# Kernel optimization log

Hardware: AMD Instinct MI355X
Metric: run time of the kernel (lower is better)

Reference implementation:

```python
import jax, jax.numpy as jnp
import numpy as np
from jax import lax

N_QUBITS = 4


def _apply_ry(state, wire, theta):
    """Apply RY(theta) on `wire`. state: [N,2,2,2,2] real. theta: scalar or [N]."""
    theta = jnp.asarray(theta)
    if theta.ndim == 1:
        theta = theta.reshape(-1, 1, 1, 1)  # broadcast over remaining qubit axes
    s = jnp.moveaxis(state, 1 + wire, -1)
    c, sn = jnp.cos(theta / 2), jnp.sin(theta / 2)
    s0, s1 = s[..., 0], s[..., 1]
    s = jnp.stack([c * s0 - sn * s1, sn * s0 + c * s1], axis=-1)
    return jnp.moveaxis(s, -1, 1 + wire)


def _apply_cnot(state, ctrl, tgt):
    s = jnp.moveaxis(state, (1 + ctrl, 1 + tgt), (-2, -1))
    s = s.at[..., 1, :].set(s[..., 1, ::-1])
    return jnp.moveaxis(s, (-2, -1), (1 + ctrl, 1 + tgt))


def _quantum_filter(patches, angles):
    """patches: [N,4] rotation angles per qubit; returns PauliZ expectations [N,4]."""
    n = patches.shape[0]
    state = jnp.zeros((n, 2, 2, 2, 2), dtype=patches.dtype)
    state = state.at[:, 0, 0, 0, 0].set(1.0)  # |0000>
    # GeneralEncoder: RY(x_i) on wire i
    for w in range(N_QUBITS):
        state = _apply_ry(state, w, patches[:, w])
    # fixed 8-op random layer: 5 RY (learned angles) + 3 CNOTs
    state = _apply_ry(state, 0, angles[0])
    state = _apply_ry(state, 1, angles[1])
    state = _apply_cnot(state, 0, 1)
    state = _apply_ry(state, 2, angles[2])
    state = _apply_cnot(state, 1, 2)
    state = _apply_ry(state, 3, angles[3])
    state = _apply_cnot(state, 2, 3)
    state = _apply_ry(state, 0, angles[4])
    # MeasureAll(PauliZ): <Z_w> = sum probs * (+1/-1 on wire w)
    probs = state * state  # real amplitudes -> |psi|^2
    z = jnp.array([1.0, -1.0], dtype=patches.dtype)
    ez = [
        (probs * z.reshape((1,) + (1,) * w + (2,) + (1,) * (N_QUBITS - 1 - w))).sum(axis=(1, 2, 3, 4))
        for w in range(N_QUBITS)
    ]
    return jnp.stack(ez, axis=-1)  # [N,4]


def setup_inputs() -> dict:
    key = jax.random.key(0)
    ks = jax.random.split(key, 6)
    B = 4096
    return {
        "x": jax.random.normal(ks[0], (B, 1, 28, 28), dtype=jnp.float32),
        "conv_w": jax.random.normal(ks[1], (4, 1, 2, 2), dtype=jnp.float32) * 0.5,
        "conv_b": jax.random.normal(ks[2], (4,), dtype=jnp.float32) * 0.1,
        "angles": jax.random.normal(ks[3], (5,), dtype=jnp.float32) * np.pi,
        "fc_w": jax.random.normal(ks[4], (10, 4 * 14 * 14), dtype=jnp.float32) * 0.03,
        "fc_b": jax.random.normal(ks[5], (10,), dtype=jnp.float32) * 0.1,
    }


def reference(x, conv_w, conv_b, angles, fc_w, fc_b):
    # classical conv: kernel 2, stride 2 -> [B,4,14,14]
    y = lax.conv_general_dilated(
        x, conv_w, window_strides=(2, 2), padding="VALID",
        dimension_numbers=("NCHW", "OIHW", "NCHW"),
    ) + conv_b[None, :, None, None]
    B, C, H, W = y.shape
    patches = y.transpose(0, 2, 3, 1).reshape(B * H * W, C)  # [B*196, 4]
    feats = _quantum_filter(patches, angles)                  # [B*196, 4]
    feats = feats.reshape(B, H * W, C).transpose(0, 2, 1).reshape(B, -1)
    logits = feats @ fc_w.T + fc_b
    return jax.nn.log_softmax(logits, axis=-1)
```

## Files before the change

### kernel.cpp

```cpp
#include <hip/hip_runtime.h>
#include <math.h>

#define NP 196
#define FEAT 784


__device__ __forceinline__ void apply_ry(float* s, const int mask, float c, float sn) {
#pragma unroll
    for (int i = 0; i < 16; ++i) {
        if (!(i & mask)) {
            float a = s[i], b = s[i | mask];
            s[i]        = c * a - sn * b;
            s[i | mask] = sn * a + c * b;
        }
    }
}

__device__ __forceinline__ void apply_cnot(float* s, const int mc, const int mt) {
#pragma unroll
    for (int i = 0; i < 16; ++i) {
        if ((i & mc) && !(i & mt)) {
            float t = s[i];
            s[i]      = s[i | mt];
            s[i | mt] = t;
        }
    }
}

__global__ void __launch_bounds__(256)
conv_quantum(const float* __restrict__ x,
             const float* __restrict__ cw,
             const float* __restrict__ cb,
             const float* __restrict__ ang,
             float* __restrict__ feats,
             int total) {
    int tid = blockIdx.x * blockDim.x + threadIdx.x;
    if (tid >= total) return;
    int b  = tid / NP;
    int hw = tid - b * NP;
    int i  = hw / 14;
    int j  = hw - i * 14;

    const float* xp = x + b * 784 + (2 * i) * 28 + 2 * j;
    float p00 = xp[0], p01 = xp[1], p10 = xp[28], p11 = xp[29];

    float cs[4], sn[4];
#pragma unroll
    for (int c = 0; c < 4; ++c) {
        float th = cw[c * 4 + 0] * p00 + cw[c * 4 + 1] * p01 +
                   cw[c * 4 + 2] * p10 + cw[c * 4 + 3] * p11 + cb[c];
        float h = 0.5f * th;
        cs[c] = __cosf(h);
        sn[c] = __sinf(h);
    }

    float s[16];
#pragma unroll
    for (int idx = 0; idx < 16; ++idx) {
        float v = (idx & 8 ? sn[0] : cs[0]);
        v      *= (idx & 4 ? sn[1] : cs[1]);
        v      *= (idx & 2 ? sn[2] : cs[2]);
        v      *= (idx & 1 ? sn[3] : cs[3]);
        s[idx] = v;
    }

    float a0 = 0.5f * ang[0], a1 = 0.5f * ang[1], a2 = 0.5f * ang[2],
          a3 = 0.5f * ang[3], a4 = 0.5f * ang[4];
    apply_ry  (s, 8, __cosf(a0), __sinf(a0));
    apply_ry  (s, 4, __cosf(a1), __sinf(a1));
    apply_cnot(s, 8, 4);
    apply_ry  (s, 2, __cosf(a2), __sinf(a2));
    apply_cnot(s, 4, 2);
    apply_ry  (s, 1, __cosf(a3), __sinf(a3));
    apply_cnot(s, 2, 1);
    apply_ry  (s, 8, __cosf(a4), __sinf(a4));

    float ez0 = 0.f, ez1 = 0.f, ez2 = 0.f, ez3 = 0.f;
#pragma unroll
    for (int idx = 0; idx < 16; ++idx) {
        float p = s[idx] * s[idx];
        ez0 += (idx & 8) ? -p : p;
        ez1 += (idx & 4) ? -p : p;
        ez2 += (idx & 2) ? -p : p;
        ez3 += (idx & 1) ? -p : p;
    }

    float* fo = feats + b * FEAT + hw;
    fo[0 * NP] = ez0;
    fo[1 * NP] = ez1;
    fo[2 * NP] = ez2;
    fo[3 * NP] = ez3;
}


__global__ void __launch_bounds__(256)
fc_lsm(const float* __restrict__ feats,
       const float* __restrict__ W,
       const float* __restrict__ bias,
       float* __restrict__ out,
       int B) {
    int gtid = blockIdx.x * blockDim.x + threadIdx.x;
    int row  = gtid >> 6;
    int lane = threadIdx.x & 63;
    if (row >= B) return;

    const float* f = feats + row * FEAT;
    float acc[10];
#pragma unroll
    for (int k = 0; k < 10; ++k) acc[k] = 0.f;

    for (int t = lane; t < FEAT; t += 64) {
        float v = f[t];
#pragma unroll
        for (int k = 0; k < 10; ++k) acc[k] = fmaf(v, W[k * FEAT + t], acc[k]);
    }

#pragma unroll
    for (int k = 0; k < 10; ++k) {
#pragma unroll
        for (int off = 32; off > 0; off >>= 1)
            acc[k] += __shfl_down(acc[k], off, 64);
    }

    if (lane == 0) {
        float l[10], m = -INFINITY;
#pragma unroll
        for (int k = 0; k < 10; ++k) {
            l[k] = acc[k] + bias[k];
            m = fmaxf(m, l[k]);
        }
        float ssum = 0.f;
#pragma unroll
        for (int k = 0; k < 10; ++k) ssum += __expf(l[k] - m);
        float ls = __logf(ssum) + m;
#pragma unroll
        for (int k = 0; k < 10; ++k) out[row * 10 + k] = l[k] - ls;
    }
}


extern "C" void kernel_launch(void* const* d_in, const int* in_sizes, int n_in,
                              void* d_out, int out_size, void* d_ws, size_t ws_size,
                              hipStream_t stream) {
    const float* x      = (const float*)d_in[0];
    const float* conv_w = (const float*)d_in[1];
    const float* conv_b = (const float*)d_in[2];
    const float* angles = (const float*)d_in[3];
    const float* fc_w   = (const float*)d_in[4];
    const float* fc_b   = (const float*)d_in[5];
    float* out = (float*)d_out;

    int B = in_sizes[0] / 784;
    float* feats = (float*)d_ws;

    int total = B * NP;
    conv_quantum<<<(total + 255) / 256, 256, 0, stream>>>(x, conv_w, conv_b, angles,
                                                          feats, total);
    fc_lsm<<<(B * 64 + 255) / 256, 256, 0, stream>>>(feats, fc_w, fc_b, out, B);
}
```

Before: 88.73 us.

## Fuse conv-quantum filter with FC and log-softmax into one per-sample kernel

Merges the two kernels into one launch where each block handles one sample. The 784 quantum features stay in shared memory instead of going through a global workspace, and the FC reduction is split across four waves and combined through shared memory. This removes the global round trip for the features and one kernel launch. In exchange, 60 of the 256 threads sit idle during the quantum phase, and the block adds two barriers. Input loads also become float2 vector loads.

```diff
diff --git a/kernel.cpp b/kernel.cpp
--- a/kernel.cpp
+++ b/kernel.cpp
@@ -28,89 +28,84 @@
 }
 
 __global__ void __launch_bounds__(256)
-conv_quantum(const float* __restrict__ x,
-             const float* __restrict__ cw,
-             const float* __restrict__ cb,
-             const float* __restrict__ ang,
-             float* __restrict__ feats,
-             int total) {
-    int tid = blockIdx.x * blockDim.x + threadIdx.x;
-    if (tid >= total) return;
-    int b  = tid / NP;
-    int hw = tid - b * NP;
-    int i  = hw / 14;
-    int j  = hw - i * 14;
+quanv_fused(const float* __restrict__ x,
+            const float* __restrict__ cw,
+            const float* __restrict__ cb,
+            const float* __restrict__ ang,
+            const float* __restrict__ W,
+            const float* __restrict__ bias,
+            float* __restrict__ out) {
+    __shared__ float feats[FEAT];
+    __shared__ float partial[4 * 10];
 
-    const float* xp = x + b * 784 + (2 * i) * 28 + 2 * j;
-    float p00 = xp[0], p01 = xp[1], p10 = xp[28], p11 = xp[29];
+    const int b   = blockIdx.x;
+    const int tid = threadIdx.x;
 
-    float cs[4], sn[4];
+    if (tid < NP) {
+        const int i = tid / 14;
+        const int j = tid - i * 14;
+
+        const float* xp = x + b * 784 + (2 * i) * 28 + 2 * j;
+        const float2 r0 = *(const float2*)(xp);
+        const float2 r1 = *(const float2*)(xp + 28);
+
+        float cs[4], sn[4];
 #pragma unroll
-    for (int c = 0; c < 4; ++c) {
-        float th = cw[c * 4 + 0] * p00 + cw[c * 4 + 1] * p01 +
-                   cw[c * 4 + 2] * p10 + cw[c * 4 + 3] * p11 + cb[c];
-        float h = 0.5f * th;
-        cs[c] = __cosf(h);
-        sn[c] = __sinf(h);
+        for (int c = 0; c < 4; ++c) {
+            float th = cw[c * 4 + 0] * r0.x + cw[c * 4 + 1] * r0.y +
+                       cw[c * 4 + 2] * r1.x + cw[c * 4 + 3] * r1.y + cb[c];
+            float h = 0.5f * th;
+            cs[c] = __cosf(h);
+            sn[c] = __sinf(h);
+        }
+
+        float s[16];
+        {
+            float v00 = cs[0] * cs[1], v01 = cs[0] * sn[1];
+            float v10 = sn[0] * cs[1], v11 = sn[0] * sn[1];
+            float w00 = cs[2] * cs[3], w01 = cs[2] * sn[3];
+            float w10 = sn[2] * cs[3], w11 = sn[2] * sn[3];
+            s[ 0] = v00 * w00; s[ 1] = v00 * w01; s[ 2] = v00 * w10; s[ 3] = v00 * w11;
+            s[ 4] = v01 * w00; s[ 5] = v01 * w01; s[ 6] = v01 * w10; s[ 7] = v01 * w11;
+            s[ 8] = v10 * w00; s[ 9] = v10 * w01; s[10] = v10 * w10; s[11] = v10 * w11;
+            s[12] = v11 * w00; s[13] = v11 * w01; s[14] = v11 * w10; s[15] = v11 * w11;
+        }
+
+        float a0 = 0.5f * ang[0], a1 = 0.5f * ang[1], a2 = 0.5f * ang[2],
+              a3 = 0.5f * ang[3], a4 = 0.5f * ang[4];
+        apply_ry  (s, 8, __cosf(a0), __sinf(a0));
+        apply_ry  (s, 4, __cosf(a1), __sinf(a1));
+        apply_cnot(s, 8, 4);
+        apply_ry  (s, 2, __cosf(a2), __sinf(a2));
+        apply_cnot(s, 4, 2);
+        apply_ry  (s, 1, __cosf(a3), __sinf(a3));
+        apply_cnot(s, 2, 1);
+        apply_ry  (s, 8, __cosf(a4), __sinf(a4));
+
+        float ez0 = 0.f, ez1 = 0.f, ez2 = 0.f, ez3 = 0.f;
+#pragma unroll
+        for (int idx = 0; idx < 16; ++idx) {
+            float p = s[idx] * s[idx];
+            ez0 += (idx & 8) ? -p : p;
+            ez1 += (idx & 4) ? -p : p;
+            ez2 += (idx & 2) ? -p : p;
+            ez3 += (idx & 1) ? -p : p;
+        }
+
+        feats[0 * NP + tid] = ez0;
+        feats[1 * NP + tid] = ez1;
+        feats[2 * NP + tid] = ez2;
+        feats[3 * NP + tid] = ez3;
     }
 
-    float s[16];
-#pragma unroll
-    for (int idx = 0; idx < 16; ++idx) {
-        float v = (idx & 8 ? sn[0] : cs[0]);
-        v      *= (idx & 4 ? sn[1] : cs[1]);
-        v      *= (idx & 2 ? sn[2] : cs[2]);
-        v      *= (idx & 1 ? sn[3] : cs[3]);
-        s[idx] = v;
-    }
+    __syncthreads();
 
-    float a0 = 0.5f * ang[0], a1 = 0.5f * ang[1], a2 = 0.5f * ang[2],
-          a3 = 0.5f * ang[3], a4 = 0.5f * ang[4];
-    apply_ry  (s, 8, __cosf(a0), __sinf(a0));
-    apply_ry  (s, 4, __cosf(a1), __sinf(a1));
-    apply_cnot(s, 8, 4);
-    apply_ry  (s, 2, __cosf(a2), __sinf(a2));
-    apply_cnot(s, 4, 2);
-    apply_ry  (s, 1, __cosf(a3), __sinf(a3));
-    apply_cnot(s, 2, 1);
-    apply_ry  (s, 8, __cosf(a4), __sinf(a4));
-
-    float ez0 = 0.f, ez1 = 0.f, ez2 = 0.f, ez3 = 0.f;
-#pragma unroll
-    for (int idx = 0; idx < 16; ++idx) {
-        float p = s[idx] * s[idx];
-        ez0 += (idx & 8) ? -p : p;
-        ez1 += (idx & 4) ? -p : p;
-        ez2 += (idx & 2) ? -p : p;
-        ez3 += (idx & 1) ? -p : p;
-    }
-
-    float* fo = feats + b * FEAT + hw;
-    fo[0 * NP] = ez0;
-    fo[1 * NP] = ez1;
-    fo[2 * NP] = ez2;
-    fo[3 * NP] = ez3;
-}
-
-
-__global__ void __launch_bounds__(256)
-fc_lsm(const float* __restrict__ feats,
-       const float* __restrict__ W,
-       const float* __restrict__ bias,
-       float* __restrict__ out,
-       int B) {
-    int gtid = blockIdx.x * blockDim.x + threadIdx.x;
-    int row  = gtid >> 6;
-    int lane = threadIdx.x & 63;
-    if (row >= B) return;
-
-    const float* f = feats + row * FEAT;
     float acc[10];
 #pragma unroll
     for (int k = 0; k < 10; ++k) acc[k] = 0.f;
 
-    for (int t = lane; t < FEAT; t += 64) {
-        float v = f[t];
+    for (int t = tid; t < FEAT; t += 256) {
+        float v = feats[t];
 #pragma unroll
         for (int k = 0; k < 10; ++k) acc[k] = fmaf(v, W[k * FEAT + t], acc[k]);
     }
@@ -121,23 +116,30 @@
         for (int off = 32; off > 0; off >>= 1)
             acc[k] += __shfl_down(acc[k], off, 64);
     }
+    const int wave = tid >> 6;
+    const int lane = tid & 63;
+    if (lane == 0) {
+#pragma unroll
+        for (int k = 0; k < 10; ++k) partial[wave * 10 + k] = acc[k];
+    }
+    __syncthreads();
 
-    if (lane == 0) {
+    if (tid == 0) {
         float l[10], m = -INFINITY;
 #pragma unroll
         for (int k = 0; k < 10; ++k) {
-            l[k] = acc[k] + bias[k];
+            l[k] = partial[k] + partial[10 + k] + partial[20 + k] + partial[30 + k] + bias[k];
             m = fmaxf(m, l[k]);
         }
         float ssum = 0.f;
 #pragma unroll
         for (int k = 0; k < 10; ++k) ssum += __expf(l[k] - m);
         float ls = __logf(ssum) + m;
+        float* o = out + b * 10;
 #pragma unroll
-        for (int k = 0; k < 10; ++k) out[row * 10 + k] = l[k] - ls;
+        for (int k = 0; k < 10; ++k) o[k] = l[k] - ls;
     }
 }
-
 
 extern "C" void kernel_launch(void* const* d_in, const int* in_sizes, int n_in,
                               void* d_out, int out_size, void* d_ws, size_t ws_size,
@@ -151,10 +153,5 @@
     float* out = (float*)d_out;
 
     int B = in_sizes[0] / 784;
-    float* feats = (float*)d_ws;
-
-    int total = B * NP;
-    conv_quantum<<<(total + 255) / 256, 256, 0, stream>>>(x, conv_w, conv_b, angles,
-                                                          feats, total);
-    fc_lsm<<<(B * 64 + 255) / 256, 256, 0, stream>>>(feats, fc_w, fc_b, out, B);
+    quanv_fused<<<B, 256, 0, stream>>>(x, conv_w, conv_b, angles, fc_w, fc_b, out);
 }
```

Result: faster. 82.79 us (-6.7%).
